# Optimization experiments

Measured on AMD Instinct MI355X. Metric: run time of the kernel, lower is better.

Reference implementation:

```python
import jax, jax.numpy as jnp
import numpy as np

N = 50000      # num nodes
E = 800000     # num edges (avg degree 16)
F_IN = 64      # num_node_features
H = 128        # hidden_channels (GatedGraphConv out_channels)
C = 16         # num_classes
L = 3          # num_layers


def setup_inputs() -> dict:
    key = jax.random.key(0)
    ks = jax.random.split(key, 9)
    s = 0.05
    x = jax.random.normal(ks[0], (N, F_IN), dtype=jnp.float32)
    edge_index = jax.random.randint(ks[1], (2, E), 0, N, dtype=jnp.int64)
    # GatedGraphConv per-layer message weights [L, H, H]
    W = jax.random.normal(ks[2], (L, H, H), dtype=jnp.float32) * s
    # GRUCell params (torch layout: rows ordered [r, z, n])
    w_ih = jax.random.normal(ks[3], (3 * H, H), dtype=jnp.float32) * s
    w_hh = jax.random.normal(ks[4], (3 * H, H), dtype=jnp.float32) * s
    b_ih = jax.random.normal(ks[5], (3 * H,), dtype=jnp.float32) * s
    b_hh = jax.random.normal(ks[6], (3 * H,), dtype=jnp.float32) * s
    # final classifier
    lin_w = jax.random.normal(ks[7], (C, H), dtype=jnp.float32) * s
    lin_b = jax.random.normal(ks[8], (C,), dtype=jnp.float32) * s
    return {"x": x, "edge_index": edge_index, "W": W, "w_ih": w_ih,
            "w_hh": w_hh, "b_ih": b_ih, "b_hh": b_hh,
            "lin_w": lin_w, "lin_b": lin_b}


def _gru_cell(m, h, w_ih, w_hh, b_ih, b_hh):
    # torch.nn.GRUCell: gates ordered r, z, n
    gi = m @ w_ih.T + b_ih   # [N, 3H]
    gh = h @ w_hh.T + b_hh   # [N, 3H]
    ir, iz, in_ = jnp.split(gi, 3, axis=1)
    hr, hz, hn = jnp.split(gh, 3, axis=1)
    r = jax.nn.sigmoid(ir + hr)
    z = jax.nn.sigmoid(iz + hz)
    n = jnp.tanh(in_ + r * hn)
    return (1.0 - z) * n + z * h


def reference(x, edge_index, W, w_ih, w_hh, b_ih, b_hh, lin_w, lin_b):
    # GatedGraphConv: zero-pad x to out_channels
    h = jnp.pad(x, ((0, 0), (0, H - F_IN)))  # [N, H]
    src = edge_index[0]  # message source (x_j)
    dst = edge_index[1]  # aggregation target
    for i in range(L):  # small fixed layer count
        m = h @ W[i]                                      # [N, H]
        agg = jax.ops.segment_sum(m[src], dst, num_segments=N)  # scatter-add
        h = _gru_cell(agg, h, w_ih, w_hh, b_ih, b_hh)
    out = h @ lin_w.T + lin_b                             # [N, C]
    return jax.nn.log_softmax(out, axis=1)
```

## Files before the change

kernel.cpp:

```cpp
#include <hip/hip_runtime.h>
#include <hip/hip_bf16.h>
#include <math.h>

#define H 128

typedef __bf16 bf16x8 __attribute__((ext_vector_type(8)));
typedef float f32x4 __attribute__((ext_vector_type(4)));
typedef __hip_bfloat16 bf16;

__device__ __forceinline__ bf16x8 ldb8(const bf16* p) {
  return *(const bf16x8*)(const void*)p;
}
__device__ __forceinline__ float fsig(float x) {
  return __fdividef(1.f, 1.f + __expf(-x));
}
__device__ __forceinline__ float ftanh(float x) {
  float x2 = fminf(fmaxf(2.f * x, -80.f), 80.f);
  float t = __expf(x2);
  return __fdividef(t - 1.f, t + 1.f);
}

__global__ __launch_bounds__(256) void k_prep(const float* __restrict__ x,
                                              bf16* __restrict__ hb,
                                              const float* __restrict__ whh,
                                              bf16* __restrict__ whhb,
                                              const float* __restrict__ W,
                                              const float* __restrict__ wih,
                                              bf16* __restrict__ G,
                                              int* __restrict__ deg, int N) {
  int i = blockIdx.x * 256 + threadIdx.x;
  int NH_ = N * H;
  if (i < NH_) {
    int f = i & (H - 1);
    int n = i >> 7;
    hb[i] = __float2bfloat16((f < 64) ? x[n * 64 + f] : 0.f);
    return;
  }
  i -= NH_;
  if (i < 3 * H * H) {
    whhb[i] = __float2bfloat16(whh[i]);
    return;
  }
  i -= 3 * H * H;
  if (i < 3 * 3 * H * H) {
    int l = i / (3 * H * H);
    int r = i % (3 * H * H);
    int j = r >> 7;
    int k = r & (H - 1);
    const float4* a = (const float4*)(wih + (size_t)j * H);
    const float4* b = (const float4*)(W + (size_t)l * H * H + (size_t)k * H);
    float s = 0.f;
#pragma unroll
    for (int q = 0; q < 32; q++) {
      float4 av = a[q], bv = b[q];
      s += av.x * bv.x + av.y * bv.y + av.z * bv.z + av.w * bv.w;
    }
    G[i] = __float2bfloat16(s);
    return;
  }
  i -= 3 * 3 * H * H;
  if (i < N) deg[i] = 0;
}

__global__ __launch_bounds__(256) void k_count(const int* __restrict__ dst,
                                               int* __restrict__ deg, int E) {
  int e = blockIdx.x * 256 + threadIdx.x;
  if (e < E) atomicAdd(&deg[dst[e]], 1);
}

__global__ __launch_bounds__(256) void k_bsum(const int* __restrict__ deg,
                                              int* __restrict__ bsums, int N) {
  __shared__ int ws[4];
  int t = threadIdx.x;
  int i = blockIdx.x * 256 + t;
  int v = (i < N) ? deg[i] : 0;
#pragma unroll
  for (int d = 1; d < 64; d <<= 1) v += __shfl_xor(v, d, 64);
  if ((t & 63) == 0) ws[t >> 6] = v;
  __syncthreads();
  if (t == 0) bsums[blockIdx.x] = ws[0] + ws[1] + ws[2] + ws[3];
}

__global__ __launch_bounds__(256) void k_bscan(int* __restrict__ bsums, int nb) {
  __shared__ int ws[4];
  int t = threadIdx.x;
  int lane = t & 63, w = t >> 6;
  int v = (t < nb) ? bsums[t] : 0;
  int s = v;
#pragma unroll
  for (int d = 1; d < 64; d <<= 1) {
    int u = __shfl_up(s, d, 64);
    if (lane >= d) s += u;
  }
  if (lane == 63) ws[w] = s;
  __syncthreads();
  int woff = 0;
  if (w >= 1) woff += ws[0];
  if (w >= 2) woff += ws[1];
  if (w >= 3) woff += ws[2];
  if (t < nb) bsums[t] = woff + s - v;
}

__global__ __launch_bounds__(256) void k_scan2(const int* __restrict__ deg,
                                               const int* __restrict__ bsums,
                                               int* __restrict__ rowptr,
                                               int* __restrict__ cursor,
                                               int N, int E) {
  __shared__ int ws[4];
  int t = threadIdx.x;
  int lane = t & 63, w = t >> 6;
  int i = blockIdx.x * 256 + t;
  int v = (i < N) ? deg[i] : 0;
  int s = v;
#pragma unroll
  for (int d = 1; d < 64; d <<= 1) {
    int u = __shfl_up(s, d, 64);
    if (lane >= d) s += u;
  }
  if (lane == 63) ws[w] = s;
  __syncthreads();
  int woff = 0;
  if (w >= 1) woff += ws[0];
  if (w >= 2) woff += ws[1];
  if (w >= 3) woff += ws[2];
  int excl = bsums[blockIdx.x] + woff + s - v;
  if (i < N) { rowptr[i] = excl; cursor[i] = excl; }
  if (i == 0) rowptr[N] = E;
}

__global__ __launch_bounds__(256) void k_fill(const int* __restrict__ src,
                                              const int* __restrict__ dst,
                                              int* __restrict__ cursor,
                                              int* __restrict__ csr_src, int E) {
  int e = blockIdx.x * 256 + threadIdx.x;
  if (e < E) {
    int pos = atomicAdd(&cursor[dst[e]], 1);
    csr_src[pos] = src[e];
  }
}

#define ASTRIDE 136
#define FSTRIDE 132
__global__ __launch_bounds__(512) void k_layer(const bf16* __restrict__ hbin,
                                               bf16* __restrict__ hbout,
                                               const bf16* __restrict__ Gl,
                                               const bf16* __restrict__ whhb,
                                               const float* __restrict__ bih,
                                               const float* __restrict__ bhh,
                                               const int* __restrict__ rowptr,
                                               const int* __restrict__ csr_src,
                                               const float* __restrict__ lw,
                                               const float* __restrict__ lb,
                                               float* __restrict__ out,
                                               int N) {
  __shared__ bf16 As[32 * ASTRIDE];
  __shared__ bf16 Hs[32 * ASTRIDE];
  __shared__ float Sf[32 * FSTRIDE];
  int t = threadIdx.x;
  int w = t >> 6;
  int lane = t & 63;
  int row0 = blockIdx.x * 32;

  {
    int rl = t >> 4;
    int cc = t & 15;
    int row = row0 + rl; if (row > N - 1) row = N - 1;
    *(bf16x8*)(&Hs[rl * ASTRIDE + cc * 8]) = ldb8(hbin + (size_t)row * H + cc * 8);
  }

  int base = row0 + w * 4;
  int rp[5];
#pragma unroll
  for (int j = 0; j < 5; j++) {
    int rw = base + j; if (rw > N) rw = N;
    rp[j] = rowptr[rw];
  }

  int e4 = lane >> 4;
  int c = lane & 15;
#pragma unroll
  for (int rr = 0; rr < 4; rr++) {
    int row = base + rr;
    float acc[8];
#pragma unroll
    for (int j = 0; j < 8; j++) acc[j] = 0.f;
    if (row < N) {
      int rb = rp[rr], re = rp[rr + 1];
      for (int b0 = rb; b0 < re; b0 += 64) {
        int n = re - b0; if (n > 64) n = 64;
        int idx = (lane < n) ? csr_src[b0 + lane] : 0;
        int nf = n & ~15;
        for (int s = e4; s < nf; s += 16) {
          int i0 = __shfl(idx, s, 64);
          int i1 = __shfl(idx, s + 4, 64);
          int i2 = __shfl(idx, s + 8, 64);
          int i3 = __shfl(idx, s + 12, 64);
          bf16x8 v0 = ldb8(hbin + (size_t)i0 * H + c * 8);
          bf16x8 v1 = ldb8(hbin + (size_t)i1 * H + c * 8);
          bf16x8 v2 = ldb8(hbin + (size_t)i2 * H + c * 8);
          bf16x8 v3 = ldb8(hbin + (size_t)i3 * H + c * 8);
#pragma unroll
          for (int j = 0; j < 8; j++)
            acc[j] += ((float)v0[j] + (float)v1[j]) + ((float)v2[j] + (float)v3[j]);
        }
        if (nf < n) {
          int s0 = nf + e4;
          int i0 = __shfl(idx, (s0 < n) ? s0 : 0, 64);
          int i1 = __shfl(idx, (s0 + 4 < n) ? s0 + 4 : 0, 64);
          int i2 = __shfl(idx, (s0 + 8 < n) ? s0 + 8 : 0, 64);
          int i3 = __shfl(idx, (s0 + 12 < n) ? s0 + 12 : 0, 64);
          if (s0 < n) {
            bf16x8 v = ldb8(hbin + (size_t)i0 * H + c * 8);
#pragma unroll
            for (int j = 0; j < 8; j++) acc[j] += (float)v[j];
          }
          if (s0 + 4 < n) {
            bf16x8 v = ldb8(hbin + (size_t)i1 * H + c * 8);
#pragma unroll
            for (int j = 0; j < 8; j++) acc[j] += (float)v[j];
          }
          if (s0 + 8 < n) {
            bf16x8 v = ldb8(hbin + (size_t)i2 * H + c * 8);
#pragma unroll
            for (int j = 0; j < 8; j++) acc[j] += (float)v[j];
          }
          if (s0 + 12 < n) {
            bf16x8 v = ldb8(hbin + (size_t)i3 * H + c * 8);
#pragma unroll
            for (int j = 0; j < 8; j++) acc[j] += (float)v[j];
          }
        }
      }
    }
#pragma unroll
    for (int j = 0; j < 8; j++) {
      acc[j] += __shfl_xor(acc[j], 16, 64);
      acc[j] += __shfl_xor(acc[j], 32, 64);
    }
    if (e4 == 0) {
      int rl = w * 4 + rr;
      bf16x8 o;
#pragma unroll
      for (int j = 0; j < 8; j++) o[j] = (__bf16)acc[j];
      *(bf16x8*)(&As[rl * ASTRIDE + c * 8]) = o;
    }
  }
  __syncthreads();

  int r = lane & 15, quad = lane >> 4, laneK = quad * 8;
  int col = w * 16 + r;

  f32x4 aIR[2], aIZ[2], aIN[2], aHR[2], aHZ[2], aHN[2];
#pragma unroll
  for (int q = 0; q < 2; q++) {
    aIR[q] = (f32x4){0.f, 0.f, 0.f, 0.f};
    aIZ[q] = aIR[q]; aIN[q] = aIR[q];
    aHR[q] = aIR[q]; aHZ[q] = aIR[q]; aHN[q] = aIR[q];
  }

  size_t wo0 = (size_t)(0 * H + col) * H;
  size_t wo1 = (size_t)(1 * H + col) * H;
  size_t wo2 = (size_t)(2 * H + col) * H;

#pragma unroll
  for (int kb = 0; kb < 4; kb++) {
    int ko = kb * 32 + laneK;
    bf16x8 a0 = *(const bf16x8*)(&As[r * ASTRIDE + ko]);
    bf16x8 a1 = *(const bf16x8*)(&As[(16 + r) * ASTRIDE + ko]);
    bf16x8 h0 = *(const bf16x8*)(&Hs[r * ASTRIDE + ko]);
    bf16x8 h1 = *(const bf16x8*)(&Hs[(16 + r) * ASTRIDE + ko]);
    bf16x8 gr = ldb8(Gl + wo0 + ko);
    aIR[0] = __builtin_amdgcn_mfma_f32_16x16x32_bf16(a0, gr, aIR[0], 0, 0, 0);
    aIR[1] = __builtin_amdgcn_mfma_f32_16x16x32_bf16(a1, gr, aIR[1], 0, 0, 0);
    bf16x8 gz = ldb8(Gl + wo1 + ko);
    aIZ[0] = __builtin_amdgcn_mfma_f32_16x16x32_bf16(a0, gz, aIZ[0], 0, 0, 0);
    aIZ[1] = __builtin_amdgcn_mfma_f32_16x16x32_bf16(a1, gz, aIZ[1], 0, 0, 0);
    bf16x8 gn = ldb8(Gl + wo2 + ko);
    aIN[0] = __builtin_amdgcn_mfma_f32_16x16x32_bf16(a0, gn, aIN[0], 0, 0, 0);
    aIN[1] = __builtin_amdgcn_mfma_f32_16x16x32_bf16(a1, gn, aIN[1], 0, 0, 0);
    bf16x8 ur = ldb8(whhb + wo0 + ko);
    aHR[0] = __builtin_amdgcn_mfma_f32_16x16x32_bf16(h0, ur, aHR[0], 0, 0, 0);
    aHR[1] = __builtin_amdgcn_mfma_f32_16x16x32_bf16(h1, ur, aHR[1], 0, 0, 0);
    bf16x8 uz = ldb8(whhb + wo1 + ko);
    aHZ[0] = __builtin_amdgcn_mfma_f32_16x16x32_bf16(h0, uz, aHZ[0], 0, 0, 0);
    aHZ[1] = __builtin_amdgcn_mfma_f32_16x16x32_bf16(h1, uz, aHZ[1], 0, 0, 0);
    bf16x8 un = ldb8(whhb + wo2 + ko);
    aHN[0] = __builtin_amdgcn_mfma_f32_16x16x32_bf16(h0, un, aHN[0], 0, 0, 0);
    aHN[1] = __builtin_amdgcn_mfma_f32_16x16x32_bf16(h1, un, aHN[1], 0, 0, 0);
  }

  float bir = bih[col], biz = bih[H + col], bin = bih[2 * H + col];
  float bhr = bhh[col], bhz = bhh[H + col], bhn = bhh[2 * H + col];
  bf16* Sb = (bf16*)Sf;
#pragma unroll
  for (int q = 0; q < 2; q++) {
#pragma unroll
    for (int i = 0; i < 4; i++) {
      int lrow = q * 16 + quad * 4 + i;
      int row = row0 + lrow;
      if (row < N) {
        float rg = fsig(aIR[q][i] + bir + aHR[q][i] + bhr);
        float zg = fsig(aIZ[q][i] + biz + aHZ[q][i] + bhz);
        float ng = ftanh(aIN[q][i] + bin + rg * (aHN[q][i] + bhn));
        float hold = __bfloat162float(Hs[lrow * ASTRIDE + col]);
        float hp = (1.f - zg) * ng + zg * hold;
        if (out) Sf[lrow * FSTRIDE + col] = hp;
        else Sb[lrow * ASTRIDE + col] = __float2bfloat16(hp);
      }
    }
  }
  __syncthreads();

  if (!out) {
    int rl = t >> 4;
    int cc = t & 15;
    int row = row0 + rl;
    if (row < N) {
      bf16x8 v = *(const bf16x8*)(&Sb[rl * ASTRIDE + cc * 8]);
      *(bf16x8*)(hbout + (size_t)row * H + cc * 8) = v;
    }
  } else {
    int cc = lane & 15;
    int q2 = lane >> 4;
    f32x4 wv[8];
    const float* wrow = lw + (size_t)cc * H + q2 * 32;
#pragma unroll
    for (int k = 0; k < 8; k++) wv[k] = *(const f32x4*)(wrow + k * 4);
    float bias = lb[cc];
#pragma unroll
    for (int rr = 0; rr < 4; rr++) {
      int lrow = w * 4 + rr;
      int row = row0 + lrow;
      if (row >= N) continue;
      const float* hrow = &Sf[lrow * FSTRIDE + q2 * 32];
      float p = 0.f;
#pragma unroll
      for (int k = 0; k < 8; k++) {
        f32x4 hv = *(const f32x4*)(hrow + k * 4);
        p += hv[0] * wv[k][0] + hv[1] * wv[k][1] + hv[2] * wv[k][2] + hv[3] * wv[k][3];
      }
      p += __shfl_xor(p, 16, 64);
      p += __shfl_xor(p, 32, 64);
      float z = p + bias;
      float mx = z;
#pragma unroll
      for (int d = 1; d < 16; d <<= 1) mx = fmaxf(mx, __shfl_xor(mx, d, 64));
      float e = expf(z - mx);
      float ssum = e;
#pragma unroll
      for (int d = 1; d < 16; d <<= 1) ssum += __shfl_xor(ssum, d, 64);
      if (q2 == 0) out[(size_t)row * 16 + cc] = z - mx - logf(ssum);
    }
  }
}

extern "C" void kernel_launch(void* const* d_in, const int* in_sizes, int n_in,
                              void* d_out, int out_size, void* d_ws, size_t ws_size,
                              hipStream_t stream) {
  const float* x   = (const float*)d_in[0];
  const int*   ei  = (const int*)d_in[1];
  const float* W   = (const float*)d_in[2];
  const float* wih = (const float*)d_in[3];
  const float* whh = (const float*)d_in[4];
  const float* bih = (const float*)d_in[5];
  const float* bhh = (const float*)d_in[6];
  const float* lw  = (const float*)d_in[7];
  const float* lb  = (const float*)d_in[8];
  float* out = (float*)d_out;

  int N = in_sizes[0] / 64;
  int E = in_sizes[1] / 2;
  const int* src = ei;
  const int* dst = ei + E;

  size_t NH = (size_t)N * H;
  bf16* hb0  = (bf16*)d_ws;
  bf16* hb1  = hb0 + NH;
  bf16* Gb   = hb1 + NH;
  bf16* whhb = Gb + 3 * 3 * H * H;
  int* deg     = (int*)(whhb + 3 * H * H);
  int* rowptr  = deg + N;
  int* cursor  = rowptr + N + 1;
  int* bsums   = cursor + N;
  int* csr_src = bsums + 256;

  int nb_e = (E + 255) / 256;
  int nb_n = (N + 255) / 256;

  int totalPrep = (int)NH + 3 * H * H + 3 * 3 * H * H + N;
  k_prep<<<(totalPrep + 255) / 256, 256, 0, stream>>>(x, hb0, whh, whhb, W, wih,
                                                      Gb, deg, N);
  k_count<<<nb_e, 256, 0, stream>>>(dst, deg, E);
  k_bsum<<<nb_n, 256, 0, stream>>>(deg, bsums, N);
  k_bscan<<<1, 256, 0, stream>>>(bsums, nb_n);
  k_scan2<<<nb_n, 256, 0, stream>>>(deg, bsums, rowptr, cursor, N, E);
  k_fill<<<nb_e, 256, 0, stream>>>(src, dst, cursor, csr_src, E);

  int nb_layer = (N + 31) / 32;
  bf16* hbp[2] = {hb0, hb1};
  for (int l = 0; l < 3; l++) {
    bf16* hin  = hbp[l & 1];
    bf16* hout = hbp[(l + 1) & 1];
    k_layer<<<nb_layer, 512, 0, stream>>>(hin, hout, Gb + (size_t)l * 3 * H * H,
                                          whhb, bih, bhh, rowptr, csr_src,
                                          lw, lb, (l == 2) ? out : nullptr, N);
  }
}
```

Baseline: 452.6 us.

## Batch neighbor gathers across rows, shrink LDS, fuse degree count into prep

```diff
diff --git a/kernel.cpp b/kernel.cpp
--- a/kernel.cpp
+++ b/kernel.cpp
@@ -10,6 +10,9 @@
 
 __device__ __forceinline__ bf16x8 ldb8(const bf16* p) {
   return *(const bf16x8*)(const void*)p;
+}
+__device__ __forceinline__ bf16x8 ldb8o(const bf16* base, unsigned byteoff) {
+  return *(const bf16x8*)(const void*)((const char*)base + byteoff);
 }
 __device__ __forceinline__ float fsig(float x) {
   return __fdividef(1.f, 1.f + __expf(-x));
@@ -27,7 +30,9 @@
                                               const float* __restrict__ W,
                                               const float* __restrict__ wih,
                                               bf16* __restrict__ G,
-                                              int* __restrict__ deg, int N) {
+                                              const int* __restrict__ dst,
+                                              int* __restrict__ deg,
+                                              int N, int E) {
   int i = blockIdx.x * 256 + threadIdx.x;
   int NH_ = N * H;
   if (i < NH_) {
@@ -59,13 +64,7 @@
     return;
   }
   i -= 3 * 3 * H * H;
-  if (i < N) deg[i] = 0;
-}
-
-__global__ __launch_bounds__(256) void k_count(const int* __restrict__ dst,
-                                               int* __restrict__ deg, int E) {
-  int e = blockIdx.x * 256 + threadIdx.x;
-  if (e < E) atomicAdd(&deg[dst[e]], 1);
+  if (i < E) atomicAdd(&deg[dst[i]], 1);
 }
 
 __global__ __launch_bounds__(256) void k_bsum(const int* __restrict__ deg,
@@ -153,12 +152,12 @@
                                                const float* __restrict__ lb,
                                                float* __restrict__ out,
                                                int N) {
-  __shared__ bf16 As[32 * ASTRIDE];
-  __shared__ bf16 Hs[32 * ASTRIDE];
-  __shared__ float Sf[32 * FSTRIDE];
+  __shared__ bf16 SH[64 * ASTRIDE];
+  bf16* As = SH;
+  bf16* Hs = SH + 32 * ASTRIDE;
   int t = threadIdx.x;
-  int w = t >> 6;
   int lane = t & 63;
+  int wu = __builtin_amdgcn_readfirstlane(t >> 6);
   int row0 = blockIdx.x * 32;
 
   {
@@ -168,7 +167,7 @@
     *(bf16x8*)(&Hs[rl * ASTRIDE + cc * 8]) = ldb8(hbin + (size_t)row * H + cc * 8);
   }
 
-  int base = row0 + w * 4;
+  int base = row0 + wu * 4;
   int rp[5];
 #pragma unroll
   for (int j = 0; j < 5; j++) {
@@ -178,77 +177,91 @@
 
   int e4 = lane >> 4;
   int c = lane & 15;
+  unsigned coff = (unsigned)c << 4;
+
+  int idxr[4];
 #pragma unroll
   for (int rr = 0; rr < 4; rr++) {
-    int row = base + rr;
-    float acc[8];
-#pragma unroll
-    for (int j = 0; j < 8; j++) acc[j] = 0.f;
-    if (row < N) {
+    int rb = rp[rr];
+    int n = rp[rr + 1] - rb; if (n > 64) n = 64;
+    idxr[rr] = (lane < n) ? csr_src[rb + lane] : 0;
+  }
+
+  float acc[4][8];
+#pragma unroll
+  for (int rr = 0; rr < 4; rr++)
+#pragma unroll
+    for (int j = 0; j < 8; j++) acc[rr][j] = 0.f;
+
+#pragma unroll
+  for (int rr = 0; rr < 4; rr++) {
+    int n = rp[rr + 1] - rp[rr];
+    bf16x8 vv[8];
+    float sc[8];
+#pragma unroll
+    for (int k = 0; k < 8; k++) {
+      int s = e4 + 4 * k;
+      int on = s < n;
+      int ie = __shfl(idxr[rr], on ? s : 0, 64);
+      vv[k] = ldb8o(hbin, ((unsigned)ie << 8) | coff);
+      sc[k] = on ? 1.f : 0.f;
+    }
+#pragma unroll
+    for (int k = 0; k < 8; k++) {
+#pragma unroll
+      for (int j = 0; j < 8; j++)
+        acc[rr][j] = fmaf(sc[k], (float)vv[k][j], acc[rr][j]);
+    }
+    if (n > 32) {
+      int hi = (n < 64) ? n : 64;
+      for (int s0 = 32; s0 < hi; s0 += 4) {
+        int s = s0 + e4;
+        int on = s < hi;
+        int ie = __shfl(idxr[rr], on ? s : 0, 64);
+        bf16x8 v = ldb8o(hbin, ((unsigned)ie << 8) | coff);
+        float scl = on ? 1.f : 0.f;
+#pragma unroll
+        for (int j = 0; j < 8; j++) acc[rr][j] = fmaf(scl, (float)v[j], acc[rr][j]);
+      }
       int rb = rp[rr], re = rp[rr + 1];
-      for (int b0 = rb; b0 < re; b0 += 64) {
-        int n = re - b0; if (n > 64) n = 64;
-        int idx = (lane < n) ? csr_src[b0 + lane] : 0;
-        int nf = n & ~15;
-        for (int s = e4; s < nf; s += 16) {
-          int i0 = __shfl(idx, s, 64);
-          int i1 = __shfl(idx, s + 4, 64);
-          int i2 = __shfl(idx, s + 8, 64);
-          int i3 = __shfl(idx, s + 12, 64);
-          bf16x8 v0 = ldb8(hbin + (size_t)i0 * H + c * 8);
-          bf16x8 v1 = ldb8(hbin + (size_t)i1 * H + c * 8);
-          bf16x8 v2 = ldb8(hbin + (size_t)i2 * H + c * 8);
-          bf16x8 v3 = ldb8(hbin + (size_t)i3 * H + c * 8);
-#pragma unroll
-          for (int j = 0; j < 8; j++)
-            acc[j] += ((float)v0[j] + (float)v1[j]) + ((float)v2[j] + (float)v3[j]);
-        }
-        if (nf < n) {
-          int s0 = nf + e4;
-          int i0 = __shfl(idx, (s0 < n) ? s0 : 0, 64);
-          int i1 = __shfl(idx, (s0 + 4 < n) ? s0 + 4 : 0, 64);
-          int i2 = __shfl(idx, (s0 + 8 < n) ? s0 + 8 : 0, 64);
-          int i3 = __shfl(idx, (s0 + 12 < n) ? s0 + 12 : 0, 64);
-          if (s0 < n) {
-            bf16x8 v = ldb8(hbin + (size_t)i0 * H + c * 8);
-#pragma unroll
-            for (int j = 0; j < 8; j++) acc[j] += (float)v[j];
-          }
-          if (s0 + 4 < n) {
-            bf16x8 v = ldb8(hbin + (size_t)i1 * H + c * 8);
-#pragma unroll
-            for (int j = 0; j < 8; j++) acc[j] += (float)v[j];
-          }
-          if (s0 + 8 < n) {
-            bf16x8 v = ldb8(hbin + (size_t)i2 * H + c * 8);
-#pragma unroll
-            for (int j = 0; j < 8; j++) acc[j] += (float)v[j];
-          }
-          if (s0 + 12 < n) {
-            bf16x8 v = ldb8(hbin + (size_t)i3 * H + c * 8);
-#pragma unroll
-            for (int j = 0; j < 8; j++) acc[j] += (float)v[j];
-          }
+      for (int b0 = rb + 64; b0 < re; b0 += 64) {
+        int n2 = re - b0; if (n2 > 64) n2 = 64;
+        int idx2 = (lane < n2) ? csr_src[b0 + lane] : 0;
+        for (int s0 = 0; s0 < n2; s0 += 4) {
+          int s = s0 + e4;
+          int on = s < n2;
+          int ie = __shfl(idx2, on ? s : 0, 64);
+          bf16x8 v = ldb8o(hbin, ((unsigned)ie << 8) | coff);
+          float scl = on ? 1.f : 0.f;
+#pragma unroll
+          for (int j = 0; j < 8; j++) acc[rr][j] = fmaf(scl, (float)v[j], acc[rr][j]);
         }
       }
     }
+  }
+
+#pragma unroll
+  for (int rr = 0; rr < 4; rr++) {
 #pragma unroll
     for (int j = 0; j < 8; j++) {
-      acc[j] += __shfl_xor(acc[j], 16, 64);
-      acc[j] += __shfl_xor(acc[j], 32, 64);
+      acc[rr][j] += __shfl_xor(acc[rr][j], 16, 64);
+      acc[rr][j] += __shfl_xor(acc[rr][j], 32, 64);
     }
     if (e4 == 0) {
-      int rl = w * 4 + rr;
+      int rl = wu * 4 + rr;
       bf16x8 o;
 #pragma unroll
-      for (int j = 0; j < 8; j++) o[j] = (__bf16)acc[j];
+      for (int j = 0; j < 8; j++) o[j] = (__bf16)acc[rr][j];
       *(bf16x8*)(&As[rl * ASTRIDE + c * 8]) = o;
     }
   }
   __syncthreads();
 
   int r = lane & 15, quad = lane >> 4, laneK = quad * 8;
-  int col = w * 16 + r;
+  unsigned col = (unsigned)(wu * 16 + r);
+  unsigned wg0 = col << 8;
+  unsigned wg1 = (1u << 15) | wg0;
+  unsigned wg2 = (2u << 15) | wg0;
 
   f32x4 aIR[2], aIZ[2], aIN[2], aHR[2], aHZ[2], aHN[2];
 #pragma unroll
@@ -258,55 +271,60 @@
     aHR[q] = aIR[q]; aHZ[q] = aIR[q]; aHN[q] = aIR[q];
   }
 
-  size_t wo0 = (size_t)(0 * H + col) * H;
-  size_t wo1 = (size_t)(1 * H + col) * H;
-  size_t wo2 = (size_t)(2 * H + col) * H;
-
 #pragma unroll
   for (int kb = 0; kb < 4; kb++) {
     int ko = kb * 32 + laneK;
+    unsigned ko2 = (unsigned)(ko << 1);
     bf16x8 a0 = *(const bf16x8*)(&As[r * ASTRIDE + ko]);
     bf16x8 a1 = *(const bf16x8*)(&As[(16 + r) * ASTRIDE + ko]);
     bf16x8 h0 = *(const bf16x8*)(&Hs[r * ASTRIDE + ko]);
     bf16x8 h1 = *(const bf16x8*)(&Hs[(16 + r) * ASTRIDE + ko]);
-    bf16x8 gr = ldb8(Gl + wo0 + ko);
+    bf16x8 gr = ldb8o(Gl, wg0 | ko2);
     aIR[0] = __builtin_amdgcn_mfma_f32_16x16x32_bf16(a0, gr, aIR[0], 0, 0, 0);
     aIR[1] = __builtin_amdgcn_mfma_f32_16x16x32_bf16(a1, gr, aIR[1], 0, 0, 0);
-    bf16x8 gz = ldb8(Gl + wo1 + ko);
+    bf16x8 gz = ldb8o(Gl, wg1 | ko2);
     aIZ[0] = __builtin_amdgcn_mfma_f32_16x16x32_bf16(a0, gz, aIZ[0], 0, 0, 0);
     aIZ[1] = __builtin_amdgcn_mfma_f32_16x16x32_bf16(a1, gz, aIZ[1], 0, 0, 0);
-    bf16x8 gn = ldb8(Gl + wo2 + ko);
+    bf16x8 gn = ldb8o(Gl, wg2 | ko2);
     aIN[0] = __builtin_amdgcn_mfma_f32_16x16x32_bf16(a0, gn, aIN[0], 0, 0, 0);
     aIN[1] = __builtin_amdgcn_mfma_f32_16x16x32_bf16(a1, gn, aIN[1], 0, 0, 0);
-    bf16x8 ur = ldb8(whhb + wo0 + ko);
+    bf16x8 ur = ldb8o(whhb, wg0 | ko2);
     aHR[0] = __builtin_amdgcn_mfma_f32_16x16x32_bf16(h0, ur, aHR[0], 0, 0, 0);
     aHR[1] = __builtin_amdgcn_mfma_f32_16x16x32_bf16(h1, ur, aHR[1], 0, 0, 0);
-    bf16x8 uz = ldb8(whhb + wo1 + ko);
+    bf16x8 uz = ldb8o(whhb, wg1 | ko2);
     aHZ[0] = __builtin_amdgcn_mfma_f32_16x16x32_bf16(h0, uz, aHZ[0], 0, 0, 0);
     aHZ[1] = __builtin_amdgcn_mfma_f32_16x16x32_bf16(h1, uz, aHZ[1], 0, 0, 0);
-    bf16x8 un = ldb8(whhb + wo2 + ko);
+    bf16x8 un = ldb8o(whhb, wg2 | ko2);
     aHN[0] = __builtin_amdgcn_mfma_f32_16x16x32_bf16(h0, un, aHN[0], 0, 0, 0);
     aHN[1] = __builtin_amdgcn_mfma_f32_16x16x32_bf16(h1, un, aHN[1], 0, 0, 0);
   }
 
   float bir = bih[col], biz = bih[H + col], bin = bih[2 * H + col];
   float bhr = bhh[col], bhz = bhh[H + col], bhn = bhh[2 * H + col];
-  bf16* Sb = (bf16*)Sf;
+  float hpv[2][4];
 #pragma unroll
   for (int q = 0; q < 2; q++) {
 #pragma unroll
     for (int i = 0; i < 4; i++) {
       int lrow = q * 16 + quad * 4 + i;
-      int row = row0 + lrow;
-      if (row < N) {
-        float rg = fsig(aIR[q][i] + bir + aHR[q][i] + bhr);
-        float zg = fsig(aIZ[q][i] + biz + aHZ[q][i] + bhz);
-        float ng = ftanh(aIN[q][i] + bin + rg * (aHN[q][i] + bhn));
-        float hold = __bfloat162float(Hs[lrow * ASTRIDE + col]);
-        float hp = (1.f - zg) * ng + zg * hold;
-        if (out) Sf[lrow * FSTRIDE + col] = hp;
-        else Sb[lrow * ASTRIDE + col] = __float2bfloat16(hp);
-      }
+      float rg = fsig(aIR[q][i] + bir + aHR[q][i] + bhr);
+      float zg = fsig(aIZ[q][i] + biz + aHZ[q][i] + bhz);
+      float ng = ftanh(aIN[q][i] + bin + rg * (aHN[q][i] + bhn));
+      float hold = __bfloat162float(Hs[lrow * ASTRIDE + col]);
+      hpv[q][i] = (1.f - zg) * ng + zg * hold;
+    }
+  }
+  __syncthreads();
+
+  bf16* Sb = SH;
+  float* Sf = (float*)SH;
+#pragma unroll
+  for (int q = 0; q < 2; q++) {
+#pragma unroll
+    for (int i = 0; i < 4; i++) {
+      int lrow = q * 16 + quad * 4 + i;
+      if (out) Sf[lrow * FSTRIDE + col] = hpv[q][i];
+      else Sb[lrow * ASTRIDE + col] = __float2bfloat16(hpv[q][i]);
     }
   }
   __syncthreads();
@@ -329,7 +347,7 @@
     float bias = lb[cc];
 #pragma unroll
     for (int rr = 0; rr < 4; rr++) {
-      int lrow = w * 4 + rr;
+      int lrow = wu * 4 + rr;
       int row = row0 + lrow;
       if (row >= N) continue;
       const float* hrow = &Sf[lrow * FSTRIDE + q2 * 32];
@@ -387,10 +405,10 @@
   int nb_e = (E + 255) / 256;
   int nb_n = (N + 255) / 256;
 
-  int totalPrep = (int)NH + 3 * H * H + 3 * 3 * H * H + N;
+  hipMemsetAsync(deg, 0, (size_t)N * sizeof(int), stream);
+  int totalPrep = (int)NH + 3 * H * H + 3 * 3 * H * H + E;
   k_prep<<<(totalPrep + 255) / 256, 256, 0, stream>>>(x, hb0, whh, whhb, W, wih,
-                                                      Gb, deg, N);
-  k_count<<<nb_e, 256, 0, stream>>>(dst, deg, E);
+                                                      Gb, dst, deg, N, E);
   k_bsum<<<nb_n, 256, 0, stream>>>(deg, bsums, N);
   k_bscan<<<1, 256, 0, stream>>>(bsums, nb_n);
   k_scan2<<<nb_n, 256, 0, stream>>>(deg, bsums, rowptr, cursor, N, E);
```

New measurement: 410.9 us (median of 2 runs). 9.2% less time.
